# Kernel optimization log

Hardware: AMD Instinct MI355X
Metric: run time of the kernel (lower is better)

The kernel has to match this reference:

```python
import jax, jax.numpy as jnp
import numpy as np

NE = 200000   # num_entities
NR = 16       # num_relations
D  = 128      # embed_dim
B  = 4096     # batch
S  = 64       # neighbors per node
L  = 2        # num_layers
H  = 4        # attention heads (hardcoded in module)


def _ln(x, g, b, eps=1e-5):
    m = jnp.mean(x, -1, keepdims=True)
    v = jnp.mean((x - m) ** 2, -1, keepdims=True)
    return (x - m) * jax.lax.rsqrt(v + eps) * g + b


def setup_inputs() -> dict:
    key = jax.random.key(0)
    ks = jax.random.split(key, 12)
    s = 0.05
    return {
        'drug_entity_indices': jax.random.randint(ks[0], (B,), 0, NE),
        'adj_entity': jax.random.randint(ks[1], (B, S), 0, NE),
        'adj_relation': jax.random.randint(ks[2], (B, S), 0, NR),
        'edge_weights': jax.random.uniform(ks[3], (B, S), dtype=jnp.float32),
        'entity_emb': jax.random.normal(ks[4], (NE, D), jnp.float32) * s,
        'W_rgcn': jax.random.normal(ks[5], (L, NR, D, D), jnp.float32) * s,
        'res_w': jax.random.normal(ks[6], (L, D, D), jnp.float32) * s,
        'res_b': jnp.zeros((L, D), jnp.float32),
        'proj_w': jax.random.normal(ks[7], (L, D, D), jnp.float32) * s,
        'proj_b': jnp.zeros((L, D), jnp.float32),
        'ln_g': jnp.ones((L, D), jnp.float32),
        'ln_b': jnp.zeros((L, D), jnp.float32),
        'in_proj_w': jax.random.normal(ks[8], (3 * D, D), jnp.float32) * s,
        'in_proj_b': jnp.zeros((3 * D,), jnp.float32),
        'out_proj_w': jax.random.normal(ks[9], (D, D), jnp.float32) * s,
        'out_proj_b': jnp.zeros((D,), jnp.float32),
        'fln_g': jnp.ones((D,), jnp.float32),
        'fln_b': jnp.zeros((D,), jnp.float32),
    }


def reference(drug_entity_indices, adj_entity, adj_relation, edge_weights,
              entity_emb, W_rgcn, res_w, res_b, proj_w, proj_b, ln_g, ln_b,
              in_proj_w, in_proj_b, out_proj_w, out_proj_b, fln_g, fln_b):
    node = entity_emb[drug_entity_indices]           # [B,D] combined_emb
    nbr = entity_emb[adj_entity]                     # [B,S,D]
    # Route each edge to its relation: sum_s nbr*ew*[rel==r] then one GEMM per relation
    # (mathematically identical to the per-relation masked matmul loop in torch).
    onehot = jax.nn.one_hot(adj_relation, NR, dtype=node.dtype)      # [B,S,R]
    pre = jnp.einsum('bsd,bsr->brd', nbr * edge_weights[..., None], onehot)
    outs = []
    for l in range(L):
        msgs = jnp.einsum('brd,rde->be', pre, W_rgcn[l])             # [B,D]
        h = jax.nn.relu(node + msgs + node @ res_w[l].T + res_b[l])  # RGCNAggregator
        node = _ln(h @ proj_w[l].T + proj_b[l] + node, ln_g[l], ln_b[l])
        outs.append(node)
    x = jnp.stack(outs, 0)                           # [L,B,D] seq-first
    qkv = x @ in_proj_w.T + in_proj_b
    q, k, v = jnp.split(qkv, 3, axis=-1)
    hd = D // H
    def heads(t):
        return t.reshape(L, B, H, hd).transpose(1, 2, 0, 3)          # [B,H,L,hd]
    q, k, v = heads(q), heads(k), heads(v)
    att = jax.nn.softmax(jnp.einsum('bhld,bhmd->bhlm', q, k) / np.sqrt(hd).astype(np.float32), axis=-1)
    o = jnp.einsum('bhlm,bhmd->bhld', att, v).transpose(2, 0, 1, 3).reshape(L, B, D)
    o = o @ out_proj_w.T + out_proj_b
    return _ln(o.mean(0), fln_g, fln_b)              # [B,D]
```

## Files before the change

kernel.cpp:

```cpp
#include <hip/hip_runtime.h>
#include <math.h>

#define NRREL 16
#define DDIM 128
#define BBATCH 4096
#define SNBR 64

typedef __attribute__((ext_vector_type(8))) short short8;
typedef __attribute__((ext_vector_type(4))) float floatx4;

__device__ __forceinline__ unsigned short f2bf(float f) {
    unsigned u = __builtin_bit_cast(unsigned, f);
    u += 0x7fffu + ((u >> 16) & 1u);
    return (unsigned short)(u >> 16);
}
__device__ __forceinline__ float bf2f(unsigned short u) {
    return __builtin_bit_cast(float, ((unsigned)u) << 16);
}

extern "C" __global__ __launch_bounds__(128)
void k_gather(const int* __restrict__ drug, const int* __restrict__ adj_e,
              const int* __restrict__ adj_r, const float* __restrict__ ew,
              const float* __restrict__ emb,
              unsigned short* __restrict__ pre_bf,
              float* __restrict__ node_f, unsigned short* __restrict__ node_bf)
{
    const int b = blockIdx.x, t = threadIdx.x;
    const int g = t >> 5, c = t & 31;
    __shared__ float pre4[4 * NRREL * DDIM];
    #pragma unroll
    for (int i = t; i < 4 * NRREL * DDIM; i += 128) pre4[i] = 0.f;
    __syncthreads();

    const int base = b * SNBR;
    float* myacc = pre4 + g * (NRREL * DDIM) + 4 * c;
    #pragma unroll 4
    for (int i = 0; i < SNBR / 4; ++i) {
        int s = 4 * i + g;
        int e = adj_e[base + s];
        int r = adj_r[base + s];
        float w = ew[base + s];
        float4 v = *(const float4*)(emb + (size_t)e * DDIM + 4 * c);
        float* p = myacc + r * DDIM;
        p[0] = fmaf(v.x, w, p[0]);
        p[1] = fmaf(v.y, w, p[1]);
        p[2] = fmaf(v.z, w, p[2]);
        p[3] = fmaf(v.w, w, p[3]);
    }
    if (t < 32) {
        float4 nf = *(const float4*)(emb + (size_t)drug[b] * DDIM + 4 * t);
        *(float4*)(node_f + (size_t)b * DDIM + 4 * t) = nf;
        ushort4 nb = { f2bf(nf.x), f2bf(nf.y), f2bf(nf.z), f2bf(nf.w) };
        *(ushort4*)(node_bf + (size_t)b * DDIM + 4 * t) = nb;
    }
    __syncthreads();
    #pragma unroll
    for (int idx = t; idx < NRREL * DDIM; idx += 128) {
        float v = pre4[idx] + pre4[2048 + idx] + pre4[4096 + idx] + pre4[6144 + idx];
        pre_bf[(size_t)b * 2048 + idx] = f2bf(v);
    }
}

extern "C" __global__ __launch_bounds__(256)
void k_wconv(const float* __restrict__ W_rgcn, const float* __restrict__ res_w,
             const float* __restrict__ proj_w, const float* __restrict__ in_w,
             const float* __restrict__ out_w,
             unsigned short* __restrict__ Wcat, unsigned short* __restrict__ resw,
             unsigned short* __restrict__ projw, unsigned short* __restrict__ inw,
             unsigned short* __restrict__ outw)
{
    int i = blockIdx.x * 256 + threadIdx.x;
    if (i < 524288) {
        int n = i >> 11, k = i & 2047;
        int l = n >> 7, e = n & 127;
        Wcat[i] = f2bf(W_rgcn[((size_t)l * 2048 + k) * 128 + e]);
    } else {
        int j = i - 524288;
        if (j < 32768)       resw[j] = f2bf(res_w[j]);
        else if (j < 65536)  projw[j - 32768] = f2bf(proj_w[j - 32768]);
        else if (j < 114688) inw[j - 65536] = f2bf(in_w[j - 65536]);
        else                 outw[j - 114688] = f2bf(out_w[j - 114688]);
    }
}

extern "C" __global__ __launch_bounds__(256)
void k_msgs(const unsigned short* __restrict__ pre_bf,
            const unsigned short* __restrict__ Wcat, float* __restrict__ msgs)
{
    int wave = threadIdx.x >> 6, wm = wave >> 1, wn = wave & 1;
    int r0 = blockIdx.x * 64 + wm * 32;
    int c0 = blockIdx.y * 64 + wn * 32;
    int lane = threadIdx.x & 63, l15 = lane & 15, q = lane >> 4;
    floatx4 acc[2][2] = {};
    const unsigned short* a0 = pre_bf + (size_t)(r0 + l15) * 2048 + q * 8;
    const unsigned short* a1 = a0 + (size_t)16 * 2048;
    const unsigned short* b0 = Wcat + (size_t)(c0 + l15) * 2048 + q * 8;
    const unsigned short* b1 = b0 + (size_t)16 * 2048;
    #pragma unroll 2
    for (int k = 0; k < 2048; k += 32) {
        short8 A0 = *(const short8*)(a0 + k);
        short8 A1 = *(const short8*)(a1 + k);
        short8 B0 = *(const short8*)(b0 + k);
        short8 B1 = *(const short8*)(b1 + k);
        acc[0][0] = __builtin_amdgcn_mfma_f32_16x16x32_bf16(A0, B0, acc[0][0], 0, 0, 0);
        acc[0][1] = __builtin_amdgcn_mfma_f32_16x16x32_bf16(A0, B1, acc[0][1], 0, 0, 0);
        acc[1][0] = __builtin_amdgcn_mfma_f32_16x16x32_bf16(A1, B0, acc[1][0], 0, 0, 0);
        acc[1][1] = __builtin_amdgcn_mfma_f32_16x16x32_bf16(A1, B1, acc[1][1], 0, 0, 0);
    }
    for (int mi = 0; mi < 2; ++mi)
        for (int ni = 0; ni < 2; ++ni) {
            int gc = c0 + ni * 16 + l15;
            #pragma unroll
            for (int r = 0; r < 4; ++r) {
                int gr = r0 + mi * 16 + 4 * q + r;
                msgs[(size_t)gr * 256 + gc] = acc[mi][ni][r];
            }
        }
}

extern "C" __global__ __launch_bounds__(256)
void k_layer(const unsigned short* __restrict__ resw, const unsigned short* __restrict__ projw,
             const float* __restrict__ res_b, const float* __restrict__ proj_b,
             const float* __restrict__ ln_g, const float* __restrict__ ln_b,
             const float* __restrict__ msgs,
             float* __restrict__ node_f, unsigned short* __restrict__ node_bf,
             unsigned short* __restrict__ xs_bf, int l)
{
    __shared__ unsigned short h_lds[64][136];
    const int t = threadIdx.x, w = t >> 6, lane = t & 63, l15 = lane & 15, q = lane >> 4;
    const int r0 = blockIdx.x * 64;
    {
        const unsigned short* Rw = resw + (size_t)l * DDIM * DDIM;
        floatx4 acc[8] = {};
        const unsigned short* ap = node_bf + (size_t)(r0 + 16 * w + l15) * DDIM + 8 * q;
        #pragma unroll
        for (int kk = 0; kk < DDIM; kk += 32) {
            short8 A0 = *(const short8*)(ap + kk);
            #pragma unroll
            for (int ni = 0; ni < 8; ++ni) {
                short8 B = *(const short8*)(Rw + (size_t)(ni * 16 + l15) * DDIM + kk + 8 * q);
                acc[ni] = __builtin_amdgcn_mfma_f32_16x16x32_bf16(A0, B, acc[ni], 0, 0, 0);
            }
        }
        #pragma unroll
        for (int ni = 0; ni < 8; ++ni) {
            int gc = ni * 16 + l15;
            float rb = res_b[l * DDIM + gc];
            #pragma unroll
            for (int r = 0; r < 4; ++r) {
                int lr = 16 * w + 4 * q + r, gr = r0 + lr;
                float v = acc[ni][r] + rb + node_f[(size_t)gr * DDIM + gc]
                        + msgs[(size_t)gr * 256 + l * DDIM + gc];
                h_lds[lr][gc] = f2bf(v > 0.f ? v : 0.f);
            }
        }
    }
    __syncthreads();
    {
        const unsigned short* Pw = projw + (size_t)l * DDIM * DDIM;
        floatx4 acc[8] = {};
        const unsigned short* ap = &h_lds[16 * w + l15][8 * q];
        #pragma unroll
        for (int kk = 0; kk < DDIM; kk += 32) {
            short8 A0 = *(const short8*)(ap + kk);
            #pragma unroll
            for (int ni = 0; ni < 8; ++ni) {
                short8 B = *(const short8*)(Pw + (size_t)(ni * 16 + l15) * DDIM + kk + 8 * q);
                acc[ni] = __builtin_amdgcn_mfma_f32_16x16x32_bf16(A0, B, acc[ni], 0, 0, 0);
            }
        }
        float vv[4][8];
        float s[4] = {0, 0, 0, 0}, sq[4] = {0, 0, 0, 0};
        #pragma unroll
        for (int ni = 0; ni < 8; ++ni) {
            int gc = ni * 16 + l15;
            float pb = proj_b[l * DDIM + gc];
            #pragma unroll
            for (int r = 0; r < 4; ++r) {
                int gr = r0 + 16 * w + 4 * q + r;
                float v = acc[ni][r] + pb + node_f[(size_t)gr * DDIM + gc];
                vv[r][ni] = v; s[r] += v; sq[r] += v * v;
            }
        }
        #pragma unroll
        for (int r = 0; r < 4; ++r)
            #pragma unroll
            for (int off = 8; off >= 1; off >>= 1) {
                s[r] += __shfl_xor(s[r], off, 64);
                sq[r] += __shfl_xor(sq[r], off, 64);
            }
        #pragma unroll
        for (int ni = 0; ni < 8; ++ni) {
            int gc = ni * 16 + l15;
            float g = ln_g[l * DDIM + gc], bb = ln_b[l * DDIM + gc];
            #pragma unroll
            for (int r = 0; r < 4; ++r) {
                int gr = r0 + 16 * w + 4 * q + r;
                float mean = s[r] * (1.f / DDIM);
                float var = sq[r] * (1.f / DDIM) - mean * mean;
                float val = (vv[r][ni] - mean) * rsqrtf(var + 1e-5f) * g + bb;
                node_f[(size_t)gr * DDIM + gc] = val;
                unsigned short vb = f2bf(val);
                node_bf[(size_t)gr * DDIM + gc] = vb;
                xs_bf[(size_t)(2 * gr + l) * DDIM + gc] = vb;
            }
        }
    }
}

extern "C" __global__ __launch_bounds__(256)
void k_head(const unsigned short* __restrict__ xs_bf, const unsigned short* __restrict__ inw,
            const float* __restrict__ in_b, const unsigned short* __restrict__ outw,
            const float* __restrict__ out_b, const float* __restrict__ fg,
            const float* __restrict__ fb, float* __restrict__ outp)
{
    __shared__ unsigned short qkv_lds[64][392];
    __shared__ unsigned short o_lds[64][136];
    const int t = threadIdx.x, w = t >> 6, lane = t & 63, l15 = lane & 15, q = lane >> 4;
    const int r0 = blockIdx.x * 64;
    {
        floatx4 acc[24] = {};
        const unsigned short* ap = xs_bf + (size_t)(r0 + 16 * w + l15) * DDIM + 8 * q;
        #pragma unroll
        for (int kk = 0; kk < DDIM; kk += 32) {
            short8 A0 = *(const short8*)(ap + kk);
            #pragma unroll
            for (int ni = 0; ni < 24; ++ni) {
                short8 B = *(const short8*)(inw + (size_t)(ni * 16 + l15) * DDIM + kk + 8 * q);
                acc[ni] = __builtin_amdgcn_mfma_f32_16x16x32_bf16(A0, B, acc[ni], 0, 0, 0);
            }
        }
        #pragma unroll
        for (int ni = 0; ni < 24; ++ni) {
            int gc = ni * 16 + l15;
            float ib = in_b[gc];
            #pragma unroll
            for (int r = 0; r < 4; ++r)
                qkv_lds[16 * w + 4 * q + r][gc] = f2bf(acc[ni][r] + ib);
        }
    }
    __syncthreads();
    {
        int g = t >> 3, j = t & 7;
        const unsigned short* row0 = qkv_lds[2 * g];
        const unsigned short* row1 = qkv_lds[2 * g + 1];
        float p00 = 0.f, p01 = 0.f, p10 = 0.f, p11 = 0.f;
        #pragma unroll
        for (int dd = 0; dd < 16; ++dd) {
            int d = 16 * j + dd;
            float q0 = bf2f(row0[d]), k0 = bf2f(row0[128 + d]);
            float q1 = bf2f(row1[d]), k1 = bf2f(row1[128 + d]);
            p00 = fmaf(q0, k0, p00); p01 = fmaf(q0, k1, p01);
            p10 = fmaf(q1, k0, p10); p11 = fmaf(q1, k1, p11);
        }
        p00 += __shfl_xor(p00, 1, 64); p01 += __shfl_xor(p01, 1, 64);
        p10 += __shfl_xor(p10, 1, 64); p11 += __shfl_xor(p11, 1, 64);
        const float sc = 0.17677669529663687f;
        p00 *= sc; p01 *= sc; p10 *= sc; p11 *= sc;
        float m0 = fmaxf(p00, p01), e00 = expf(p00 - m0), e01 = expf(p01 - m0);
        float i0 = 1.f / (e00 + e01);
        float m1 = fmaxf(p10, p11), e10 = expf(p10 - m1), e11 = expf(p11 - m1);
        float i1 = 1.f / (e10 + e11);
        #pragma unroll
        for (int dd = 0; dd < 16; ++dd) {
            int d = 16 * j + dd;
            float v0 = bf2f(row0[256 + d]), v1 = bf2f(row1[256 + d]);
            o_lds[2 * g][d]     = f2bf((e00 * v0 + e01 * v1) * i0);
            o_lds[2 * g + 1][d] = f2bf((e10 * v0 + e11 * v1) * i1);
        }
    }
    __syncthreads();
    {
        floatx4 acc[8] = {};
        const unsigned short* ap = &o_lds[16 * w + l15][8 * q];
        #pragma unroll
        for (int kk = 0; kk < DDIM; kk += 32) {
            short8 A0 = *(const short8*)(ap + kk);
            #pragma unroll
            for (int ni = 0; ni < 8; ++ni) {
                short8 B = *(const short8*)(outw + (size_t)(ni * 16 + l15) * DDIM + kk + 8 * q);
                acc[ni] = __builtin_amdgcn_mfma_f32_16x16x32_bf16(A0, B, acc[ni], 0, 0, 0);
            }
        }
        float av[2][8];
        float s[2] = {0, 0}, sq[2] = {0, 0};
        #pragma unroll
        for (int ni = 0; ni < 8; ++ni) {
            int gc = ni * 16 + l15;
            float ob = out_b[gc];
            #pragma unroll
            for (int rr = 0; rr < 2; ++rr) {
                float v = 0.5f * (acc[ni][2 * rr] + acc[ni][2 * rr + 1]) + ob;
                av[rr][ni] = v; s[rr] += v; sq[rr] += v * v;
            }
        }
        #pragma unroll
        for (int rr = 0; rr < 2; ++rr)
            #pragma unroll
            for (int off = 8; off >= 1; off >>= 1) {
                s[rr] += __shfl_xor(s[rr], off, 64);
                sq[rr] += __shfl_xor(sq[rr], off, 64);
            }
        #pragma unroll
        for (int ni = 0; ni < 8; ++ni) {
            int gc = ni * 16 + l15;
            float g = fg[gc], bb = fb[gc];
            #pragma unroll
            for (int rr = 0; rr < 2; ++rr) {
                int bg = blockIdx.x * 32 + 8 * w + 2 * q + rr;
                float mean = s[rr] * (1.f / DDIM);
                float var = sq[rr] * (1.f / DDIM) - mean * mean;
                outp[(size_t)bg * DDIM + gc] = (av[rr][ni] - mean) * rsqrtf(var + 1e-5f) * g + bb;
            }
        }
    }
}

extern "C" void kernel_launch(void* const* d_in, const int* in_sizes, int n_in,
                              void* d_out, int out_size, void* d_ws, size_t ws_size,
                              hipStream_t stream) {
    const int*   drug_idx = (const int*)d_in[0];
    const int*   adj_ent  = (const int*)d_in[1];
    const int*   adj_rel  = (const int*)d_in[2];
    const float* ew       = (const float*)d_in[3];
    const float* emb      = (const float*)d_in[4];
    const float* W_rgcn   = (const float*)d_in[5];
    const float* res_w    = (const float*)d_in[6];
    const float* res_b    = (const float*)d_in[7];
    const float* proj_w   = (const float*)d_in[8];
    const float* proj_b   = (const float*)d_in[9];
    const float* ln_g     = (const float*)d_in[10];
    const float* ln_b     = (const float*)d_in[11];
    const float* in_w     = (const float*)d_in[12];
    const float* in_b     = (const float*)d_in[13];
    const float* out_w    = (const float*)d_in[14];
    const float* out_b    = (const float*)d_in[15];
    const float* fg       = (const float*)d_in[16];
    const float* fb       = (const float*)d_in[17];
    float* outp = (float*)d_out;

    char* ws = (char*)d_ws;
    size_t off = 0;
    auto alloc = [&](size_t bytes) { size_t o = off; off = (off + bytes + 255) & ~(size_t)255; return o; };
    unsigned short* pre_bf  = (unsigned short*)(ws + alloc((size_t)BBATCH * 2048 * 2));
    float*          node_f  = (float*)         (ws + alloc((size_t)BBATCH * 128 * 4));
    unsigned short* node_bf = (unsigned short*)(ws + alloc((size_t)BBATCH * 128 * 2));
    unsigned short* xs_bf   = (unsigned short*)(ws + alloc((size_t)2 * BBATCH * 128 * 2));
    float*          msgs    = (float*)         (ws + alloc((size_t)BBATCH * 256 * 4));
    unsigned short* Wcat    = (unsigned short*)(ws + alloc((size_t)256 * 2048 * 2));
    unsigned short* resw    = (unsigned short*)(ws + alloc((size_t)2 * 128 * 128 * 2));
    unsigned short* projw   = (unsigned short*)(ws + alloc((size_t)2 * 128 * 128 * 2));
    unsigned short* inw     = (unsigned short*)(ws + alloc((size_t)384 * 128 * 2));
    unsigned short* outw    = (unsigned short*)(ws + alloc((size_t)128 * 128 * 2));

    hipLaunchKernelGGL(k_wconv, dim3(2560), dim3(256), 0, stream,
                       W_rgcn, res_w, proj_w, in_w, out_w, Wcat, resw, projw, inw, outw);
    hipLaunchKernelGGL(k_gather, dim3(BBATCH), dim3(128), 0, stream,
                       drug_idx, adj_ent, adj_rel, ew, emb, pre_bf, node_f, node_bf);
    hipLaunchKernelGGL(k_msgs, dim3(64, 4), dim3(256), 0, stream, pre_bf, Wcat, msgs);
    for (int l = 0; l < 2; ++l)
        hipLaunchKernelGGL(k_layer, dim3(64), dim3(256), 0, stream,
                           resw, projw, res_b, proj_b, ln_g, ln_b, msgs,
                           node_f, node_bf, xs_bf, l);
    hipLaunchKernelGGL(k_head, dim3(128), dim3(256), 0, stream,
                       xs_bf, inw, in_b, outw, out_b, fg, fb, outp);
}
```

Before: 279.3 us.

## Fuse layers and head into one tail kernel, split-K msgs GEMM, restructure gather

The two per-layer kernels and the attention head are fused into one k_tail kernel that keeps node state, hidden activations and qkv in LDS across both layers. The message GEMM is split four ways along K, and the tail kernel sums the partial results. The gather now stages scaled neighbor rows in LDS and reduces per relation with no atomics-style accumulation. The weight conversion uses a tiled LDS transpose with vectorized conversions. This cuts launches, global round-trips and the low-occupancy (64-block) msgs grid, at the cost of more LDS per block and extra partial-sum traffic.

```diff
diff --git a/kernel.cpp b/kernel.cpp
--- a/kernel.cpp
+++ b/kernel.cpp
@@ -16,49 +16,6 @@
 }
 __device__ __forceinline__ float bf2f(unsigned short u) {
     return __builtin_bit_cast(float, ((unsigned)u) << 16);
-}
-
-extern "C" __global__ __launch_bounds__(128)
-void k_gather(const int* __restrict__ drug, const int* __restrict__ adj_e,
-              const int* __restrict__ adj_r, const float* __restrict__ ew,
-              const float* __restrict__ emb,
-              unsigned short* __restrict__ pre_bf,
-              float* __restrict__ node_f, unsigned short* __restrict__ node_bf)
-{
-    const int b = blockIdx.x, t = threadIdx.x;
-    const int g = t >> 5, c = t & 31;
-    __shared__ float pre4[4 * NRREL * DDIM];
-    #pragma unroll
-    for (int i = t; i < 4 * NRREL * DDIM; i += 128) pre4[i] = 0.f;
-    __syncthreads();
-
-    const int base = b * SNBR;
-    float* myacc = pre4 + g * (NRREL * DDIM) + 4 * c;
-    #pragma unroll 4
-    for (int i = 0; i < SNBR / 4; ++i) {
-        int s = 4 * i + g;
-        int e = adj_e[base + s];
-        int r = adj_r[base + s];
-        float w = ew[base + s];
-        float4 v = *(const float4*)(emb + (size_t)e * DDIM + 4 * c);
-        float* p = myacc + r * DDIM;
-        p[0] = fmaf(v.x, w, p[0]);
-        p[1] = fmaf(v.y, w, p[1]);
-        p[2] = fmaf(v.z, w, p[2]);
-        p[3] = fmaf(v.w, w, p[3]);
-    }
-    if (t < 32) {
-        float4 nf = *(const float4*)(emb + (size_t)drug[b] * DDIM + 4 * t);
-        *(float4*)(node_f + (size_t)b * DDIM + 4 * t) = nf;
-        ushort4 nb = { f2bf(nf.x), f2bf(nf.y), f2bf(nf.z), f2bf(nf.w) };
-        *(ushort4*)(node_bf + (size_t)b * DDIM + 4 * t) = nb;
-    }
-    __syncthreads();
-    #pragma unroll
-    for (int idx = t; idx < NRREL * DDIM; idx += 128) {
-        float v = pre4[idx] + pre4[2048 + idx] + pre4[4096 + idx] + pre4[6144 + idx];
-        pre_bf[(size_t)b * 2048 + idx] = f2bf(v);
-    }
 }
 
 extern "C" __global__ __launch_bounds__(256)
@@ -69,35 +26,106 @@
              unsigned short* __restrict__ projw, unsigned short* __restrict__ inw,
              unsigned short* __restrict__ outw)
 {
-    int i = blockIdx.x * 256 + threadIdx.x;
-    if (i < 524288) {
-        int n = i >> 11, k = i & 2047;
-        int l = n >> 7, e = n & 127;
-        Wcat[i] = f2bf(W_rgcn[((size_t)l * 2048 + k) * 128 + e]);
+    const int bid = blockIdx.x, t = threadIdx.x;
+    if (bid < 64) {
+        __shared__ float tileT[128 * 65];
+        const int l = bid >> 5, k0 = (bid & 31) * 64;
+        #pragma unroll
+        for (int i = 0; i < 8; ++i) {
+            int flat = t + 256 * i;
+            int k = flat >> 5, c = flat & 31;
+            float4 v = *(const float4*)(W_rgcn + ((size_t)(l * 2048 + k0 + k)) * 128 + 4 * c);
+            tileT[(4 * c + 0) * 65 + k] = v.x;
+            tileT[(4 * c + 1) * 65 + k] = v.y;
+            tileT[(4 * c + 2) * 65 + k] = v.z;
+            tileT[(4 * c + 3) * 65 + k] = v.w;
+        }
+        __syncthreads();
+        const int e = t >> 1, half = t & 1;
+        #pragma unroll
+        for (int m = 0; m < 4; ++m) {
+            int kk = 32 * half + 8 * m;
+            short8 o;
+            #pragma unroll
+            for (int j = 0; j < 8; ++j) o[j] = (short)f2bf(tileT[e * 65 + kk + j]);
+            *(short8*)(Wcat + ((size_t)(l * 128 + e)) * 2048 + k0 + kk) = o;
+        }
     } else {
-        int j = i - 524288;
-        if (j < 32768)       resw[j] = f2bf(res_w[j]);
-        else if (j < 65536)  projw[j - 32768] = f2bf(proj_w[j - 32768]);
-        else if (j < 114688) inw[j - 65536] = f2bf(in_w[j - 65536]);
-        else                 outw[j - 114688] = f2bf(out_w[j - 114688]);
-    }
+        int j4 = (bid - 64) * 1024 + t * 4;
+        const float* src; unsigned short* dst; int off;
+        if (j4 < 32768)       { src = res_w;  dst = resw;  off = j4; }
+        else if (j4 < 65536)  { src = proj_w; dst = projw; off = j4 - 32768; }
+        else if (j4 < 114688) { src = in_w;   dst = inw;   off = j4 - 65536; }
+        else                  { src = out_w;  dst = outw;  off = j4 - 114688; }
+        float4 v = *(const float4*)(src + off);
+        ushort4 o = { f2bf(v.x), f2bf(v.y), f2bf(v.z), f2bf(v.w) };
+        *(ushort4*)(dst + off) = o;
+    }
+}
+
+extern "C" __global__ __launch_bounds__(256)
+void k_gather(const int* __restrict__ drug, const int* __restrict__ adj_e,
+              const int* __restrict__ adj_r, const float* __restrict__ ew,
+              const float* __restrict__ emb,
+              unsigned short* __restrict__ pre_bf, float* __restrict__ node_f)
+{
+    __shared__ float rows[64 * 132];
+    __shared__ int   srel[64];
+    __shared__ float swt[64];
+    __shared__ int   sent[64];
+    const int b = blockIdx.x, t = threadIdx.x;
+    if (t < 64) {
+        sent[t] = adj_e[b * SNBR + t];
+        srel[t] = adj_r[b * SNBR + t];
+        swt[t]  = ew[b * SNBR + t];
+    }
+    __syncthreads();
+    #pragma unroll
+    for (int i = 0; i < 8; ++i) {
+        int flat = t + 256 * i;
+        int s = flat >> 5, c = flat & 31;
+        float w = swt[s];
+        float4 v = *(const float4*)(emb + (size_t)sent[s] * DDIM + 4 * c);
+        float4 sv; sv.x = v.x * w; sv.y = v.y * w; sv.z = v.z * w; sv.w = v.w * w;
+        *(float4*)(rows + s * 132 + 4 * c) = sv;
+    }
+    if (t < 32) {
+        float4 nf = *(const float4*)(emb + (size_t)drug[b] * DDIM + 4 * t);
+        *(float4*)(node_f + (size_t)b * DDIM + 4 * t) = nf;
+    }
+    __syncthreads();
+    const int r = t >> 4, g = t & 15;
+    float acc[8] = {0.f, 0.f, 0.f, 0.f, 0.f, 0.f, 0.f, 0.f};
+    #pragma unroll 4
+    for (int s = 0; s < SNBR; ++s) {
+        if (srel[s] == r) {
+            const float* p = rows + s * 132 + 8 * g;
+            #pragma unroll
+            for (int j = 0; j < 8; ++j) acc[j] += p[j];
+        }
+    }
+    short8 o;
+    #pragma unroll
+    for (int j = 0; j < 8; ++j) o[j] = (short)f2bf(acc[j]);
+    *(short8*)(pre_bf + (size_t)b * 2048 + r * DDIM + 8 * g) = o;
 }
 
 extern "C" __global__ __launch_bounds__(256)
 void k_msgs(const unsigned short* __restrict__ pre_bf,
-            const unsigned short* __restrict__ Wcat, float* __restrict__ msgs)
+            const unsigned short* __restrict__ Wcat, float* __restrict__ part)
 {
-    int wave = threadIdx.x >> 6, wm = wave >> 1, wn = wave & 1;
-    int r0 = blockIdx.x * 64 + wm * 32;
-    int c0 = blockIdx.y * 64 + wn * 32;
-    int lane = threadIdx.x & 63, l15 = lane & 15, q = lane >> 4;
+    const int wave = threadIdx.x >> 6, wm = wave >> 1, wn = wave & 1;
+    const int r0 = blockIdx.x * 64 + wm * 32;
+    const int c0 = blockIdx.y * 64 + wn * 32;
+    const int koff = blockIdx.z * 512;
+    const int lane = threadIdx.x & 63, l15 = lane & 15, q = lane >> 4;
     floatx4 acc[2][2] = {};
-    const unsigned short* a0 = pre_bf + (size_t)(r0 + l15) * 2048 + q * 8;
+    const unsigned short* a0 = pre_bf + (size_t)(r0 + l15) * 2048 + koff + q * 8;
     const unsigned short* a1 = a0 + (size_t)16 * 2048;
-    const unsigned short* b0 = Wcat + (size_t)(c0 + l15) * 2048 + q * 8;
+    const unsigned short* b0 = Wcat + (size_t)(c0 + l15) * 2048 + koff + q * 8;
     const unsigned short* b1 = b0 + (size_t)16 * 2048;
     #pragma unroll 2
-    for (int k = 0; k < 2048; k += 32) {
+    for (int k = 0; k < 512; k += 32) {
         short8 A0 = *(const short8*)(a0 + k);
         short8 A1 = *(const short8*)(a1 + k);
         short8 B0 = *(const short8*)(b0 + k);
@@ -107,127 +135,161 @@
         acc[1][0] = __builtin_amdgcn_mfma_f32_16x16x32_bf16(A1, B0, acc[1][0], 0, 0, 0);
         acc[1][1] = __builtin_amdgcn_mfma_f32_16x16x32_bf16(A1, B1, acc[1][1], 0, 0, 0);
     }
+    float* dst = part + (size_t)blockIdx.z * BBATCH * 256;
     for (int mi = 0; mi < 2; ++mi)
         for (int ni = 0; ni < 2; ++ni) {
             int gc = c0 + ni * 16 + l15;
             #pragma unroll
             for (int r = 0; r < 4; ++r) {
                 int gr = r0 + mi * 16 + 4 * q + r;
-                msgs[(size_t)gr * 256 + gc] = acc[mi][ni][r];
+                dst[(size_t)gr * 256 + gc] = acc[mi][ni][r];
             }
         }
 }
 
 extern "C" __global__ __launch_bounds__(256)
-void k_layer(const unsigned short* __restrict__ resw, const unsigned short* __restrict__ projw,
-             const float* __restrict__ res_b, const float* __restrict__ proj_b,
-             const float* __restrict__ ln_g, const float* __restrict__ ln_b,
-             const float* __restrict__ msgs,
-             float* __restrict__ node_f, unsigned short* __restrict__ node_bf,
-             unsigned short* __restrict__ xs_bf, int l)
+void k_tail(const float* __restrict__ node_fg, const float* __restrict__ part,
+            const unsigned short* __restrict__ resw, const unsigned short* __restrict__ projw,
+            const float* __restrict__ res_b, const float* __restrict__ proj_b,
+            const float* __restrict__ ln_g, const float* __restrict__ ln_b,
+            const unsigned short* __restrict__ inw, const float* __restrict__ in_b,
+            const unsigned short* __restrict__ outw, const float* __restrict__ out_b,
+            const float* __restrict__ fg, const float* __restrict__ fb,
+            float* __restrict__ outp)
 {
-    __shared__ unsigned short h_lds[64][136];
+    __shared__ float          node_ln[32 * 132];
+    __shared__ unsigned short node_b16[32 * 136];
+    __shared__ unsigned short h_b16[32 * 136];
+    __shared__ float          msum[32 * 260];
+    __shared__ unsigned short xs_l[64 * 136];
+    __shared__ unsigned short qkvl[64 * 392];
+    __shared__ float          psum[2][32], psq[2][32];
+
     const int t = threadIdx.x, w = t >> 6, lane = t & 63, l15 = lane & 15, q = lane >> 4;
-    const int r0 = blockIdx.x * 64;
-    {
-        const unsigned short* Rw = resw + (size_t)l * DDIM * DDIM;
-        floatx4 acc[8] = {};
-        const unsigned short* ap = node_bf + (size_t)(r0 + 16 * w + l15) * DDIM + 8 * q;
-        #pragma unroll
-        for (int kk = 0; kk < DDIM; kk += 32) {
-            short8 A0 = *(const short8*)(ap + kk);
-            #pragma unroll
-            for (int ni = 0; ni < 8; ++ni) {
-                short8 B = *(const short8*)(Rw + (size_t)(ni * 16 + l15) * DDIM + kk + 8 * q);
-                acc[ni] = __builtin_amdgcn_mfma_f32_16x16x32_bf16(A0, B, acc[ni], 0, 0, 0);
-            }
-        }
-        #pragma unroll
-        for (int ni = 0; ni < 8; ++ni) {
-            int gc = ni * 16 + l15;
-            float rb = res_b[l * DDIM + gc];
-            #pragma unroll
-            for (int r = 0; r < 4; ++r) {
-                int lr = 16 * w + 4 * q + r, gr = r0 + lr;
-                float v = acc[ni][r] + rb + node_f[(size_t)gr * DDIM + gc]
-                        + msgs[(size_t)gr * 256 + l * DDIM + gc];
-                h_lds[lr][gc] = f2bf(v > 0.f ? v : 0.f);
-            }
-        }
+    const int r0 = blockIdx.x * 32;
+    const int wm = w & 1, wn = w >> 1;
+
+    #pragma unroll
+    for (int i = 0; i < 4; ++i) {
+        int flat = t + 256 * i;
+        int rr = flat >> 5, c = flat & 31;
+        float4 v = *(const float4*)(node_fg + (size_t)(r0 + rr) * DDIM + 4 * c);
+        *(float4*)(node_ln + rr * 132 + 4 * c) = v;
+        ushort4 o = { f2bf(v.x), f2bf(v.y), f2bf(v.z), f2bf(v.w) };
+        *(ushort4*)(node_b16 + rr * 136 + 4 * c) = o;
+    }
+    #pragma unroll
+    for (int i = 0; i < 8; ++i) {
+        int flat = t + 256 * i;
+        int rr = flat >> 6, c = flat & 63;
+        float4 s = {0.f, 0.f, 0.f, 0.f};
+        #pragma unroll
+        for (int kc = 0; kc < 4; ++kc) {
+            float4 v = *(const float4*)(part + ((size_t)kc * BBATCH + r0 + rr) * 256 + 4 * c);
+            s.x += v.x; s.y += v.y; s.z += v.z; s.w += v.w;
+        }
+        *(float4*)(msum + rr * 260 + 4 * c) = s;
     }
     __syncthreads();
-    {
-        const unsigned short* Pw = projw + (size_t)l * DDIM * DDIM;
-        floatx4 acc[8] = {};
-        const unsigned short* ap = &h_lds[16 * w + l15][8 * q];
-        #pragma unroll
-        for (int kk = 0; kk < DDIM; kk += 32) {
-            short8 A0 = *(const short8*)(ap + kk);
-            #pragma unroll
-            for (int ni = 0; ni < 8; ++ni) {
-                short8 B = *(const short8*)(Pw + (size_t)(ni * 16 + l15) * DDIM + kk + 8 * q);
-                acc[ni] = __builtin_amdgcn_mfma_f32_16x16x32_bf16(A0, B, acc[ni], 0, 0, 0);
-            }
-        }
-        float vv[4][8];
-        float s[4] = {0, 0, 0, 0}, sq[4] = {0, 0, 0, 0};
-        #pragma unroll
-        for (int ni = 0; ni < 8; ++ni) {
-            int gc = ni * 16 + l15;
-            float pb = proj_b[l * DDIM + gc];
-            #pragma unroll
-            for (int r = 0; r < 4; ++r) {
-                int gr = r0 + 16 * w + 4 * q + r;
-                float v = acc[ni][r] + pb + node_f[(size_t)gr * DDIM + gc];
-                vv[r][ni] = v; s[r] += v; sq[r] += v * v;
-            }
-        }
-        #pragma unroll
-        for (int r = 0; r < 4; ++r)
-            #pragma unroll
-            for (int off = 8; off >= 1; off >>= 1) {
-                s[r] += __shfl_xor(s[r], off, 64);
-                sq[r] += __shfl_xor(sq[r], off, 64);
-            }
-        #pragma unroll
-        for (int ni = 0; ni < 8; ++ni) {
-            int gc = ni * 16 + l15;
-            float g = ln_g[l * DDIM + gc], bb = ln_b[l * DDIM + gc];
-            #pragma unroll
-            for (int r = 0; r < 4; ++r) {
-                int gr = r0 + 16 * w + 4 * q + r;
-                float mean = s[r] * (1.f / DDIM);
-                float var = sq[r] * (1.f / DDIM) - mean * mean;
-                float val = (vv[r][ni] - mean) * rsqrtf(var + 1e-5f) * g + bb;
-                node_f[(size_t)gr * DDIM + gc] = val;
-                unsigned short vb = f2bf(val);
-                node_bf[(size_t)gr * DDIM + gc] = vb;
-                xs_bf[(size_t)(2 * gr + l) * DDIM + gc] = vb;
-            }
-        }
-    }
-}
-
-extern "C" __global__ __launch_bounds__(256)
-void k_head(const unsigned short* __restrict__ xs_bf, const unsigned short* __restrict__ inw,
-            const float* __restrict__ in_b, const unsigned short* __restrict__ outw,
-            const float* __restrict__ out_b, const float* __restrict__ fg,
-            const float* __restrict__ fb, float* __restrict__ outp)
-{
-    __shared__ unsigned short qkv_lds[64][392];
-    __shared__ unsigned short o_lds[64][136];
-    const int t = threadIdx.x, w = t >> 6, lane = t & 63, l15 = lane & 15, q = lane >> 4;
-    const int r0 = blockIdx.x * 64;
+
+    for (int l = 0; l < 2; ++l) {
+        {
+            const unsigned short* Bw = resw + (size_t)l * DDIM * DDIM;
+            floatx4 acc[4] = {};
+            const unsigned short* ap = node_b16 + (16 * wm + l15) * 136 + 8 * q;
+            #pragma unroll
+            for (int kk = 0; kk < DDIM; kk += 32) {
+                short8 A = *(const short8*)(ap + kk);
+                #pragma unroll
+                for (int ni = 0; ni < 4; ++ni) {
+                    short8 B = *(const short8*)(Bw + (size_t)(64 * wn + ni * 16 + l15) * DDIM + kk + 8 * q);
+                    acc[ni] = __builtin_amdgcn_mfma_f32_16x16x32_bf16(A, B, acc[ni], 0, 0, 0);
+                }
+            }
+            #pragma unroll
+            for (int ni = 0; ni < 4; ++ni) {
+                int gc = 64 * wn + ni * 16 + l15;
+                float rb = res_b[l * DDIM + gc];
+                #pragma unroll
+                for (int r = 0; r < 4; ++r) {
+                    int lr = 16 * wm + 4 * q + r;
+                    float v = acc[ni][r] + rb + node_ln[lr * 132 + gc] + msum[lr * 260 + l * DDIM + gc];
+                    h_b16[lr * 136 + gc] = f2bf(v > 0.f ? v : 0.f);
+                }
+            }
+        }
+        __syncthreads();
+        {
+            const unsigned short* Bw = projw + (size_t)l * DDIM * DDIM;
+            floatx4 acc[4] = {};
+            const unsigned short* ap = h_b16 + (16 * wm + l15) * 136 + 8 * q;
+            #pragma unroll
+            for (int kk = 0; kk < DDIM; kk += 32) {
+                short8 A = *(const short8*)(ap + kk);
+                #pragma unroll
+                for (int ni = 0; ni < 4; ++ni) {
+                    short8 B = *(const short8*)(Bw + (size_t)(64 * wn + ni * 16 + l15) * DDIM + kk + 8 * q);
+                    acc[ni] = __builtin_amdgcn_mfma_f32_16x16x32_bf16(A, B, acc[ni], 0, 0, 0);
+                }
+            }
+            float vv[4][4];
+            float s4[4] = {0, 0, 0, 0}, sq4[4] = {0, 0, 0, 0};
+            #pragma unroll
+            for (int ni = 0; ni < 4; ++ni) {
+                int gc = 64 * wn + ni * 16 + l15;
+                float pb = proj_b[l * DDIM + gc];
+                #pragma unroll
+                for (int r = 0; r < 4; ++r) {
+                    int lr = 16 * wm + 4 * q + r;
+                    float v = acc[ni][r] + pb + node_ln[lr * 132 + gc];
+                    vv[ni][r] = v; s4[r] += v; sq4[r] += v * v;
+                }
+            }
+            #pragma unroll
+            for (int r = 0; r < 4; ++r)
+                #pragma unroll
+                for (int off = 8; off >= 1; off >>= 1) {
+                    s4[r] += __shfl_xor(s4[r], off, 64);
+                    sq4[r] += __shfl_xor(sq4[r], off, 64);
+                }
+            if (l15 == 0) {
+                #pragma unroll
+                for (int r = 0; r < 4; ++r) {
+                    psum[wn][16 * wm + 4 * q + r] = s4[r];
+                    psq[wn][16 * wm + 4 * q + r] = sq4[r];
+                }
+            }
+            __syncthreads();
+            #pragma unroll
+            for (int ni = 0; ni < 4; ++ni) {
+                int gc = 64 * wn + ni * 16 + l15;
+                float g = ln_g[l * DDIM + gc], bb = ln_b[l * DDIM + gc];
+                #pragma unroll
+                for (int r = 0; r < 4; ++r) {
+                    int lr = 16 * wm + 4 * q + r;
+                    float mean = (psum[0][lr] + psum[1][lr]) * (1.f / DDIM);
+                    float var = (psq[0][lr] + psq[1][lr]) * (1.f / DDIM) - mean * mean;
+                    float val = (vv[ni][r] - mean) * rsqrtf(var + 1e-5f) * g + bb;
+                    node_ln[lr * 132 + gc] = val;
+                    unsigned short ub = f2bf(val);
+                    node_b16[lr * 136 + gc] = ub;
+                    xs_l[(2 * lr + l) * 136 + gc] = ub;
+                }
+            }
+            __syncthreads();
+        }
+    }
+
     {
         floatx4 acc[24] = {};
-        const unsigned short* ap = xs_bf + (size_t)(r0 + 16 * w + l15) * DDIM + 8 * q;
+        const unsigned short* ap = xs_l + (16 * w + l15) * 136 + 8 * q;
         #pragma unroll
         for (int kk = 0; kk < DDIM; kk += 32) {
-            short8 A0 = *(const short8*)(ap + kk);
+            short8 A = *(const short8*)(ap + kk);
             #pragma unroll
             for (int ni = 0; ni < 24; ++ni) {
                 short8 B = *(const short8*)(inw + (size_t)(ni * 16 + l15) * DDIM + kk + 8 * q);
-                acc[ni] = __builtin_amdgcn_mfma_f32_16x16x32_bf16(A0, B, acc[ni], 0, 0, 0);
+                acc[ni] = __builtin_amdgcn_mfma_f32_16x16x32_bf16(A, B, acc[ni], 0, 0, 0);
             }
         }
         #pragma unroll
@@ -236,14 +298,15 @@
             float ib = in_b[gc];
             #pragma unroll
             for (int r = 0; r < 4; ++r)
-                qkv_lds[16 * w + 4 * q + r][gc] = f2bf(acc[ni][r] + ib);
+                qkvl[(16 * w + 4 * q + r) * 392 + gc] = f2bf(acc[ni][r] + ib);
         }
     }
     __syncthreads();
+
     {
         int g = t >> 3, j = t & 7;
-        const unsigned short* row0 = qkv_lds[2 * g];
-        const unsigned short* row1 = qkv_lds[2 * g + 1];
+        const unsigned short* row0 = qkvl + (2 * g) * 392;
+        const unsigned short* row1 = qkvl + (2 * g + 1) * 392;
         float p00 = 0.f, p01 = 0.f, p10 = 0.f, p11 = 0.f;
         #pragma unroll
         for (int dd = 0; dd < 16; ++dd) {
@@ -265,21 +328,22 @@
         for (int dd = 0; dd < 16; ++dd) {
             int d = 16 * j + dd;
             float v0 = bf2f(row0[256 + d]), v1 = bf2f(row1[256 + d]);
-            o_lds[2 * g][d]     = f2bf((e00 * v0 + e01 * v1) * i0);
-            o_lds[2 * g + 1][d] = f2bf((e10 * v0 + e11 * v1) * i1);
+            xs_l[(2 * g) * 136 + d]     = f2bf((e00 * v0 + e01 * v1) * i0);
+            xs_l[(2 * g + 1) * 136 + d] = f2bf((e10 * v0 + e11 * v1) * i1);
         }
     }
     __syncthreads();
+
     {
         floatx4 acc[8] = {};
-        const unsigned short* ap = &o_lds[16 * w + l15][8 * q];
+        const unsigned short* ap = xs_l + (16 * w + l15) * 136 + 8 * q;
         #pragma unroll
         for (int kk = 0; kk < DDIM; kk += 32) {
-            short8 A0 = *(const short8*)(ap + kk);
+            short8 A = *(const short8*)(ap + kk);
             #pragma unroll
             for (int ni = 0; ni < 8; ++ni) {
                 short8 B = *(const short8*)(outw + (size_t)(ni * 16 + l15) * DDIM + kk + 8 * q);
-                acc[ni] = __builtin_amdgcn_mfma_f32_16x16x32_bf16(A0, B, acc[ni], 0, 0, 0);
+                acc[ni] = __builtin_amdgcn_mfma_f32_16x16x32_bf16(A, B, acc[ni], 0, 0, 0);
             }
         }
         float av[2][8];
@@ -307,7 +371,7 @@
             float g = fg[gc], bb = fb[gc];
             #pragma unroll
             for (int rr = 0; rr < 2; ++rr) {
-                int bg = blockIdx.x * 32 + 8 * w + 2 * q + rr;
+                int bg = r0 + 8 * w + 2 * q + rr;
                 float mean = s[rr] * (1.f / DDIM);
                 float var = sq[rr] * (1.f / DDIM) - mean * mean;
                 outp[(size_t)bg * DDIM + gc] = (av[rr][ni] - mean) * rsqrtf(var + 1e-5f) * g + bb;
@@ -344,24 +408,19 @@
     auto alloc = [&](size_t bytes) { size_t o = off; off = (off + bytes + 255) & ~(size_t)255; return o; };
     unsigned short* pre_bf  = (unsigned short*)(ws + alloc((size_t)BBATCH * 2048 * 2));
     float*          node_f  = (float*)         (ws + alloc((size_t)BBATCH * 128 * 4));
-    unsigned short* node_bf = (unsigned short*)(ws + alloc((size_t)BBATCH * 128 * 2));
-    unsigned short* xs_bf   = (unsigned short*)(ws + alloc((size_t)2 * BBATCH * 128 * 2));
-    float*          msgs    = (float*)         (ws + alloc((size_t)BBATCH * 256 * 4));
+    float*          part    = (float*)         (ws + alloc((size_t)4 * BBATCH * 256 * 4));
     unsigned short* Wcat    = (unsigned short*)(ws + alloc((size_t)256 * 2048 * 2));
     unsigned short* resw    = (unsigned short*)(ws + alloc((size_t)2 * 128 * 128 * 2));
     unsigned short* projw   = (unsigned short*)(ws + alloc((size_t)2 * 128 * 128 * 2));
     unsigned short* inw     = (unsigned short*)(ws + alloc((size_t)384 * 128 * 2));
     unsigned short* outw    = (unsigned short*)(ws + alloc((size_t)128 * 128 * 2));
 
-    hipLaunchKernelGGL(k_wconv, dim3(2560), dim3(256), 0, stream,
+    hipLaunchKernelGGL(k_wconv, dim3(192), dim3(256), 0, stream,
                        W_rgcn, res_w, proj_w, in_w, out_w, Wcat, resw, projw, inw, outw);
-    hipLaunchKernelGGL(k_gather, dim3(BBATCH), dim3(128), 0, stream,
-                       drug_idx, adj_ent, adj_rel, ew, emb, pre_bf, node_f, node_bf);
-    hipLaunchKernelGGL(k_msgs, dim3(64, 4), dim3(256), 0, stream, pre_bf, Wcat, msgs);
-    for (int l = 0; l < 2; ++l)
-        hipLaunchKernelGGL(k_layer, dim3(64), dim3(256), 0, stream,
-                           resw, projw, res_b, proj_b, ln_g, ln_b, msgs,
-                           node_f, node_bf, xs_bf, l);
-    hipLaunchKernelGGL(k_head, dim3(128), dim3(256), 0, stream,
-                       xs_bf, inw, in_b, outw, out_b, fg, fb, outp);
-}
+    hipLaunchKernelGGL(k_gather, dim3(BBATCH), dim3(256), 0, stream,
+                       drug_idx, adj_ent, adj_rel, ew, emb, pre_bf, node_f);
+    hipLaunchKernelGGL(k_msgs, dim3(64, 4, 4), dim3(256), 0, stream, pre_bf, Wcat, part);
+    hipLaunchKernelGGL(k_tail, dim3(128), dim3(256), 0, stream,
+                       node_f, part, resw, projw, res_b, proj_b, ln_g, ln_b,
+                       inw, in_b, outw, out_b, fg, fb, outp);
+}
```

Result: faster. 267.3 us (-4.3%).
